# Kernel optimization log

Hardware: AMD Instinct MI355X
Metric: run time of the kernel (lower is better)

Reference implementation:

```python
import jax, jax.numpy as jnp
import numpy as np

DIM = 1024
DEPTH = 8
DIM_HEAD = 64
HEADS = 16
NUM_Q = 16
EMB = 768
OUT = 1024
FF_INNER = 4 * DIM
INNER = DIM_HEAD * HEADS  # 1024
B, N1 = 64, 577
EPS = 1e-5


def _ln(x, g, b):
    mu = jnp.mean(x, axis=-1, keepdims=True)
    var = jnp.mean((x - mu) ** 2, axis=-1, keepdims=True)
    return (x - mu) * jax.lax.rsqrt(var + EPS) * g + b


def setup_inputs() -> dict:
    key = jax.random.key(0)
    ks = jax.random.split(key, 16)
    std = 0.02
    inp = {
        'x': jax.random.normal(ks[0], (B, N1, EMB), jnp.float32),
        'queries': jax.random.normal(ks[1], (1, NUM_Q, DIM), jnp.float32) / DIM ** 0.5,
        'proj_in_w': jax.random.normal(ks[2], (EMB, DIM), jnp.float32) * std,
        'proj_in_b': jnp.zeros((DIM,), jnp.float32),
        'ln1_g': jnp.ones((DEPTH, DIM), jnp.float32),
        'ln1_b': jnp.zeros((DEPTH, DIM), jnp.float32),
        'ln2_g': jnp.ones((DEPTH, DIM), jnp.float32),
        'ln2_b': jnp.zeros((DEPTH, DIM), jnp.float32),
        'wq': jax.random.normal(ks[3], (DEPTH, DIM, INNER), jnp.float32) * std,
        'wkv': jax.random.normal(ks[4], (DEPTH, DIM, 2 * INNER), jnp.float32) * std,
        'wo': jax.random.normal(ks[5], (DEPTH, INNER, DIM), jnp.float32) * std,
        'ffln_g': jnp.ones((DEPTH, DIM), jnp.float32),
        'ffln_b': jnp.zeros((DEPTH, DIM), jnp.float32),
        'w1': jax.random.normal(ks[6], (DEPTH, DIM, FF_INNER), jnp.float32) * std,
        'w2': jax.random.normal(ks[7], (DEPTH, FF_INNER, DIM), jnp.float32) * std,
        'proj_out_w': jax.random.normal(ks[8], (DIM, OUT), jnp.float32) * std,
        'proj_out_b': jnp.zeros((OUT,), jnp.float32),
        'nout_g': jnp.ones((OUT,), jnp.float32),
        'nout_b': jnp.zeros((OUT,), jnp.float32),
    }
    return inp


def reference(x, queries, proj_in_w, proj_in_b, ln1_g, ln1_b, ln2_g, ln2_b,
              wq, wkv, wo, ffln_g, ffln_b, w1, w2,
              proj_out_w, proj_out_b, nout_g, nout_b):
    b = x.shape[0]
    xp = x @ proj_in_w + proj_in_b          # (b, n1, dim)
    latents0 = jnp.broadcast_to(queries, (b, NUM_Q, DIM))
    scale = DIM_HEAD ** -0.25               # applied to both q and k

    def layer(latents, p):
        (g1, b1, g2, b2, Wq, Wkv, Wo, gf, bf, W1, W2) = p
        xn = _ln(xp, g1, b1)                # (b, n1, dim)
        lt = _ln(latents, g2, b2)           # (b, nq, dim)
        q = lt @ Wq                         # (b, nq, inner)
        kv_in = jnp.concatenate([xn, lt], axis=1)   # (b, n1+nq, dim)
        kv = kv_in @ Wkv                    # (b, n1+nq, 2*inner)
        k, v = jnp.split(kv, 2, axis=-1)
        L = kv_in.shape[1]
        qh = q.reshape(b, NUM_Q, HEADS, DIM_HEAD).transpose(0, 2, 1, 3)
        kh = k.reshape(b, L, HEADS, DIM_HEAD).transpose(0, 2, 1, 3)
        vh = v.reshape(b, L, HEADS, DIM_HEAD).transpose(0, 2, 1, 3)
        logits = jnp.einsum('bhqd,bhkd->bhqk', qh * scale, kh * scale)
        w = jax.nn.softmax(logits.astype(jnp.float32), axis=-1).astype(logits.dtype)
        o = jnp.einsum('bhqk,bhkd->bhqd', w, vh)
        o = o.transpose(0, 2, 1, 3).reshape(b, NUM_Q, INNER) @ Wo
        latents = o + latents
        h = _ln(latents, gf, bf) @ W1
        h = jax.nn.gelu(h, approximate=False)
        latents = h @ W2 + latents
        return latents, None

    params = (ln1_g, ln1_b, ln2_g, ln2_b, wq, wkv, wo, ffln_g, ffln_b, w1, w2)
    latents, _ = jax.lax.scan(layer, latents0, params)
    out = latents @ proj_out_w + proj_out_b
    return _ln(out, nout_g, nout_b)
```

## Files before the change

### kernel.cpp

```cpp
#include <hip/hip_runtime.h>
#include <hip/hip_bf16.h>
#include <math.h>

#define DEV __device__ __forceinline__

typedef __bf16 bf16x8 __attribute__((ext_vector_type(8)));
typedef float f32x4 __attribute__((ext_vector_type(4)));
typedef unsigned short u16x8 __attribute__((ext_vector_type(8)));
typedef unsigned short u16x4 __attribute__((ext_vector_type(4)));

DEV float b2f(unsigned short u){ unsigned int i = ((unsigned int)u)<<16; float f; __builtin_memcpy(&f,&i,4); return f; }
DEV unsigned short f2b(float x){ unsigned int i; __builtin_memcpy(&i,&x,4); unsigned int r = i + 0x7FFFu + ((i>>16)&1u); return (unsigned short)(r>>16); }

DEV int swz(int row, int elem){ return row*64 + ((((elem>>3) ^ row) & 7)<<3) + (elem&7); }

enum { EPI_F32=0, EPI_GELU=2, EPI_RESF32=3 };

__global__ __launch_bounds__(512)
void gemm3(const unsigned short* __restrict__ A, const unsigned short* __restrict__ Bt,
           const float* __restrict__ bias, unsigned short* __restrict__ Out,
           int M, int N, int K, int NT)
{
    __shared__ unsigned short As[256*64];
    __shared__ unsigned short Bs[256*64];
    const int tid  = threadIdx.x;
    const int lane = tid & 63;
    const int wave = tid >> 6;
    const int wr = wave >> 2, wc = wave & 3;
    const int nb = blockIdx.x;
    const int nt = nb % NT, mt = nb / NT;

    f32x4 acc[8][4];
    #pragma unroll
    for (int m=0;m<8;m++)
      #pragma unroll
      for (int n=0;n<4;n++) acc[m][n] = f32x4{0.f,0.f,0.f,0.f};

    const unsigned short* pA[4]; const unsigned short* pB[4];
    int dA[4], dB[4];
    #pragma unroll
    for (int i=0;i<4;i++){
      int e = (i*512+tid)*8; int row = e>>6, col = e&63;
      int gr = mt*256 + row; if (gr > M-1) gr = M-1;
      pA[i] = A + (size_t)gr*K + col;
      dA[i] = swz(row,col);
      pB[i] = Bt + (size_t)(nt*256+row)*K + col;
      dB[i] = swz(row,col);
    }

    u16x8 rA[4], rB[4];
    auto issue = [&](int k0){
      #pragma unroll
      for (int i=0;i<4;i++) rA[i] = *reinterpret_cast<const u16x8*>(pA[i]+k0);
      #pragma unroll
      for (int i=0;i<4;i++) rB[i] = *reinterpret_cast<const u16x8*>(pB[i]+k0);
    };
    auto commit = [&](){
      #pragma unroll
      for (int i=0;i<4;i++) *reinterpret_cast<u16x8*>(&As[dA[i]]) = rA[i];
      #pragma unroll
      for (int i=0;i<4;i++) *reinterpret_cast<u16x8*>(&Bs[dB[i]]) = rB[i];
    };

    issue(0);
    const int nk = K / 64;
    #pragma unroll 1
    for (int kt=0; kt<nk; kt++){
      __syncthreads();
      commit();
      __syncthreads();
      if (kt+1 < nk) issue((kt+1)*64);
      #pragma unroll
      for (int kk=0; kk<2; kk++){
        bf16x8 bv[4];
        #pragma unroll
        for (int n=0;n<4;n++){
          int r = wc*64 + n*16 + (lane&15);
          bv[n] = (bf16x8)(*reinterpret_cast<const u16x8*>(&Bs[swz(r, kk*32 + (lane>>4)*8)]));
        }
        #pragma unroll
        for (int m=0;m<8;m++){
          int r = wr*128 + m*16 + (lane&15);
          bf16x8 av = (bf16x8)(*reinterpret_cast<const u16x8*>(&As[swz(r, kk*32 + (lane>>4)*8)]));
          #pragma unroll
          for (int n=0;n<4;n++)
            acc[m][n] = __builtin_amdgcn_mfma_f32_16x16x32_bf16(av, bv[n], acc[m][n], 0, 0, 0);
        }
      }
    }

    #pragma unroll
    for (int m=0;m<8;m++){
      #pragma unroll
      for (int n=0;n<4;n++){
        #pragma unroll
        for (int r=0;r<4;r++){
          int row = mt*256 + wr*128 + m*16 + (lane>>4)*4 + r;
          int col = nt*256 + wc*64 + n*16 + (lane&15);
          if (row < M){
            float v = acc[m][n][r];
            if (bias) v += bias[col];
            Out[(size_t)row*N + col] = f2b(v);
          }
        }
      }
    }
}

template<int EPI>
__global__ __launch_bounds__(256)
void gemm_sp2(const unsigned short* __restrict__ AH, const unsigned short* __restrict__ AL,
              const unsigned short* __restrict__ BH, const unsigned short* __restrict__ BL,
              const float* __restrict__ bias, const float* __restrict__ Res,
              void* __restrict__ Out, unsigned short* __restrict__ OutL,
              int M, int N, int K, int NT)
{
    constexpr int MR=2, NR=2;
    __shared__ unsigned short As[2*64*64];
    __shared__ unsigned short Bs[2*64*64];
    const int tid  = threadIdx.x;
    const int lane = tid & 63;
    const int wave = tid >> 6;
    const int wr = wave >> 1, wc = wave & 1;
    const int chunk = gridDim.x >> 3;
    const int nb = (blockIdx.x & 7)*chunk + (blockIdx.x >> 3);
    const int nt = nb % NT, mt = nb / NT;

    f32x4 acc[MR][NR];
    #pragma unroll
    for (int m=0;m<MR;m++)
      #pragma unroll
      for (int n=0;n<NR;n++) acc[m][n] = f32x4{0.f,0.f,0.f,0.f};

    const unsigned short *pA[2], *pB[2];
    int dst[2];
    #pragma unroll
    for (int i=0;i<2;i++){
      int e = (i*256+tid)*8; int row = e>>6, col = e&63;
      pA[i] = AH + (size_t)(mt*64+row)*K + col;
      pB[i] = BH + (size_t)(nt*64+row)*K + col;
      dst[i] = swz(row,col);
    }
    const size_t dAL = (size_t)(AL - AH);
    const size_t dBL = (size_t)(BL - BH);

    u16x8 rAH0[2], rAL0[2], rBH0[2], rBL0[2];
    u16x8 rAH1[2], rAL1[2], rBH1[2], rBL1[2];
    auto issue0 = [&](int k0){
      #pragma unroll
      for (int i=0;i<2;i++){
        rAH0[i] = *reinterpret_cast<const u16x8*>(pA[i]+k0);
        rAL0[i] = *reinterpret_cast<const u16x8*>(pA[i]+dAL+k0);
        rBH0[i] = *reinterpret_cast<const u16x8*>(pB[i]+k0);
        rBL0[i] = *reinterpret_cast<const u16x8*>(pB[i]+dBL+k0);
      }
    };
    auto issue1 = [&](int k0){
      #pragma unroll
      for (int i=0;i<2;i++){
        rAH1[i] = *reinterpret_cast<const u16x8*>(pA[i]+k0);
        rAL1[i] = *reinterpret_cast<const u16x8*>(pA[i]+dAL+k0);
        rBH1[i] = *reinterpret_cast<const u16x8*>(pB[i]+k0);
        rBL1[i] = *reinterpret_cast<const u16x8*>(pB[i]+dBL+k0);
      }
    };
    auto commit0 = [&](){
      #pragma unroll
      for (int i=0;i<2;i++){
        *reinterpret_cast<u16x8*>(&As[dst[i]])      = rAH0[i];
        *reinterpret_cast<u16x8*>(&As[4096+dst[i]]) = rAL0[i];
        *reinterpret_cast<u16x8*>(&Bs[dst[i]])      = rBH0[i];
        *reinterpret_cast<u16x8*>(&Bs[4096+dst[i]]) = rBL0[i];
      }
    };
    auto commit1 = [&](){
      #pragma unroll
      for (int i=0;i<2;i++){
        *reinterpret_cast<u16x8*>(&As[dst[i]])      = rAH1[i];
        *reinterpret_cast<u16x8*>(&As[4096+dst[i]]) = rAL1[i];
        *reinterpret_cast<u16x8*>(&Bs[dst[i]])      = rBH1[i];
        *reinterpret_cast<u16x8*>(&Bs[4096+dst[i]]) = rBL1[i];
      }
    };
    auto compute = [&](){
      #pragma unroll
      for (int kk=0; kk<2; kk++){
        bf16x8 ah[MR], al[MR], bh[NR], bl[NR];
        #pragma unroll
        for (int m=0;m<MR;m++){
          int a = swz(wr*32 + m*16 + (lane&15), kk*32 + (lane>>4)*8);
          ah[m] = (bf16x8)(*reinterpret_cast<const u16x8*>(&As[a]));
          al[m] = (bf16x8)(*reinterpret_cast<const u16x8*>(&As[4096 + a]));
        }
        #pragma unroll
        for (int n=0;n<NR;n++){
          int a = swz(wc*32 + n*16 + (lane&15), kk*32 + (lane>>4)*8);
          bh[n] = (bf16x8)(*reinterpret_cast<const u16x8*>(&Bs[a]));
          bl[n] = (bf16x8)(*reinterpret_cast<const u16x8*>(&Bs[4096 + a]));
        }
        #pragma unroll
        for (int m=0;m<MR;m++)
          #pragma unroll
          for (int n=0;n<NR;n++){
            acc[m][n] = __builtin_amdgcn_mfma_f32_16x16x32_bf16(ah[m], bh[n], acc[m][n], 0, 0, 0);
            acc[m][n] = __builtin_amdgcn_mfma_f32_16x16x32_bf16(ah[m], bl[n], acc[m][n], 0, 0, 0);
            acc[m][n] = __builtin_amdgcn_mfma_f32_16x16x32_bf16(al[m], bh[n], acc[m][n], 0, 0, 0);
          }
      }
    };

    const int nk = K / 64;
    issue0(0); issue1(64);
    #pragma unroll 1
    for (int kt=0; kt<nk; kt+=2){
      __syncthreads();
      commit0();
      __syncthreads();
      if (kt+2 < nk) issue0((kt+2)*64);
      compute();
      __syncthreads();
      commit1();
      __syncthreads();
      if (kt+3 < nk) issue1((kt+3)*64);
      compute();
    }

    #pragma unroll
    for (int m=0;m<MR;m++){
      #pragma unroll
      for (int n=0;n<NR;n++){
        #pragma unroll
        for (int r=0;r<4;r++){
          int row = mt*64 + wr*32 + m*16 + (lane>>4)*4 + r;
          int col = nt*64 + wc*32 + n*16 + (lane&15);
          float v = acc[m][n][r];
          if (bias) v += bias[col];
          if constexpr (EPI==EPI_GELU){
            v = 0.5f*v*(1.0f + erff(v*0.70710678118654752f));
            unsigned short hi = f2b(v);
            ((unsigned short*)Out)[(size_t)row*N + col] = hi;
            OutL[(size_t)row*N + col] = f2b(v - b2f(hi));
          } else {
            if constexpr (EPI==EPI_RESF32) v += Res[(size_t)row*N + col];
            ((float*)Out)[(size_t)row*N + col] = v;
          }
        }
      }
    }
}

enum { OM_F32=0, OM_BF16=1, OM_SPLIT=2 };
template<bool INF32, int OM, bool HASGB>
__global__ __launch_bounds__(256)
void ln_rows(const void* __restrict__ In, void* __restrict__ Out,
             unsigned short* __restrict__ OutL,
             const float* __restrict__ g, const float* __restrict__ bb)
{
  const int row = blockIdx.x;
  const int tid = threadIdx.x;
  const size_t base = (size_t)row*1024 + tid*4;
  float v[4];
  if constexpr (INF32){
    f32x4 t = *reinterpret_cast<const f32x4*>((const float*)In + base);
    v[0]=t[0]; v[1]=t[1]; v[2]=t[2]; v[3]=t[3];
  } else {
    u16x4 t = *reinterpret_cast<const u16x4*>((const unsigned short*)In + base);
    #pragma unroll
    for (int j=0;j<4;j++) v[j] = b2f(t[j]);
  }
  float s = v[0]+v[1]+v[2]+v[3];
  float q = v[0]*v[0]+v[1]*v[1]+v[2]*v[2]+v[3]*v[3];
  #pragma unroll
  for (int o=32;o>0;o>>=1){ s += __shfl_xor(s,o,64); q += __shfl_xor(q,o,64); }
  __shared__ float sm[8];
  const int wave = tid>>6, lane = tid&63;
  if (lane==0){ sm[wave] = s; sm[4+wave] = q; }
  __syncthreads();
  s = sm[0]+sm[1]+sm[2]+sm[3];
  q = sm[4]+sm[5]+sm[6]+sm[7];
  const float mean = s*(1.f/1024.f);
  const float rstd = rsqrtf(fmaxf(q*(1.f/1024.f) - mean*mean, 0.f) + 1e-5f);
  #pragma unroll
  for (int j=0;j<4;j++){
    float t2 = (v[j]-mean)*rstd;
    if constexpr (HASGB) t2 = t2*g[tid*4+j] + bb[tid*4+j];
    v[j] = t2;
  }
  if constexpr (OM==OM_F32){
    f32x4 t{v[0],v[1],v[2],v[3]};
    *reinterpret_cast<f32x4*>((float*)Out + base) = t;
  } else if constexpr (OM==OM_BF16){
    u16x4 t{f2b(v[0]),f2b(v[1]),f2b(v[2]),f2b(v[3])};
    *reinterpret_cast<u16x4*>((unsigned short*)Out + base) = t;
  } else {
    u16x4 h{f2b(v[0]),f2b(v[1]),f2b(v[2]),f2b(v[3])};
    u16x4 l{f2b(v[0]-b2f(h[0])),f2b(v[1]-b2f(h[1])),f2b(v[2]-b2f(h[2])),f2b(v[3]-b2f(h[3]))};
    *reinterpret_cast<u16x4*>((unsigned short*)Out + base) = h;
    *reinterpret_cast<u16x4*>(OutL + base) = l;
  }
}

template<bool LO>
__global__ __launch_bounds__(256)
void transpose_cvt_b(const float* __restrict__ W, const float* __restrict__ rs,
                     unsigned short* __restrict__ Wt, unsigned short* __restrict__ Wtlo,
                     int K, int N, size_t wLS, size_t tLS, int dstRowOff)
{
  const int l = blockIdx.z;
  const float* Wl = W + (size_t)l*wLS;
  __shared__ float t[32][33];
  const int tx = threadIdx.x & 31, ty = threadIdx.x >> 5;
  const int n0 = blockIdx.x*32, k0 = blockIdx.y*32;
  #pragma unroll
  for (int j=0;j<4;j++){
    int r = ty + j*8;
    float w = Wl[(size_t)(k0+r)*N + n0 + tx];
    if (rs) w *= rs[l*1024 + k0+r];
    t[r][tx] = w;
  }
  __syncthreads();
  #pragma unroll
  for (int j=0;j<4;j++){
    int r = ty + j*8;
    float w = t[tx][r];
    unsigned short hi = f2b(w);
    size_t di = (size_t)l*tLS + (size_t)(dstRowOff + n0 + r)*K + k0 + tx;
    Wt[di] = hi;
    if constexpr (LO) Wtlo[di] = f2b(w - b2f(hi));
  }
}

__global__ __launch_bounds__(256)
void biaskv_kernel(const float* __restrict__ ln1b, const float* __restrict__ wkv,
                   float* __restrict__ out)
{
  const int l = blockIdx.y;
  const int n = blockIdx.x*256 + threadIdx.x;
  const float* b1 = ln1b + l*1024;
  const float* W  = wkv + (size_t)l*1024*2048;
  float s = 0.f;
  for (int k=0;k<1024;k++) s += b1[k]*W[(size_t)k*2048 + n];
  out[l*2048 + n] = s;
}

__global__ __launch_bounds__(256)
void init_latents(const float* __restrict__ Q, float* __restrict__ L)
{
  size_t idx = ((size_t)blockIdx.x*256 + threadIdx.x)*4;
  int row = (int)(idx >> 10);
  int col = (int)(idx & 1023);
  f32x4 t = *reinterpret_cast<const f32x4*>(Q + (size_t)(row & 15)*1024 + col);
  *reinterpret_cast<f32x4*>(L + idx) = t;
}

__global__ __launch_bounds__(256)
void cvt_f32_bf16(const float* __restrict__ In, unsigned short* __restrict__ Out, size_t n4)
{
  size_t i = (size_t)blockIdx.x*256 + threadIdx.x;
  if (i >= n4) return;
  f32x4 t = *reinterpret_cast<const f32x4*>(In + i*4);
  u16x4 u{f2b(t[0]),f2b(t[1]),f2b(t[2]),f2b(t[3])};
  *reinterpret_cast<u16x4*>(Out + i*4) = u;
}

__global__ __launch_bounds__(256)
void cvt_f32b_pair(const float* __restrict__ In, unsigned short* __restrict__ Oh,
                   unsigned short* __restrict__ Ol)
{
  size_t idx = ((size_t)blockIdx.x*256 + threadIdx.x)*4;
  f32x4 t = *reinterpret_cast<const f32x4*>(In + idx);
  u16x4 h{f2b(t[0]),f2b(t[1]),f2b(t[2]),f2b(t[3])};
  u16x4 l{f2b(t[0]-b2f(h[0])),f2b(t[1]-b2f(h[1])),f2b(t[2]-b2f(h[2])),f2b(t[3]-b2f(h[3]))};
  *reinterpret_cast<u16x4*>(Oh + idx) = h;
  *reinterpret_cast<u16x4*>(Ol + idx) = l;
}

__global__ __launch_bounds__(256)
void attn_kernel(const float* __restrict__ QKVf,
                 const unsigned short* __restrict__ KVX,
                 unsigned short* __restrict__ ATTOh,
                 unsigned short* __restrict__ ATTOl)
{
  __shared__ float qs[16][64];
  __shared__ float ws[16][600];
  const int tid = threadIdx.x;
  const int bh = blockIdx.x;
  const int b = bh >> 4, h = bh & 15;

  {
    int idx = tid*4;
    int qi = idx >> 6, d = idx & 63;
    f32x4 t = *reinterpret_cast<const f32x4*>(QKVf + (size_t)(b*16+qi)*3072 + h*64 + d);
    #pragma unroll
    for (int j=0;j<4;j++) qs[qi][d+j] = 0.125f * t[j];
  }
  __syncthreads();

  for (int r = tid; r < 593; r += 256){
    float a[16];
    #pragma unroll
    for (int qi=0;qi<16;qi++) a[qi] = 0.f;
    if (r < 577){
      const unsigned short* krow = KVX + ((size_t)(b*577 + r)*2048 + h*64);
      #pragma unroll 4
      for (int d4=0; d4<16; d4++){
        u16x4 k4 = *reinterpret_cast<const u16x4*>(krow + d4*4);
        float kf0=b2f(k4[0]), kf1=b2f(k4[1]), kf2=b2f(k4[2]), kf3=b2f(k4[3]);
        #pragma unroll
        for (int qi=0;qi<16;qi++){
          f32x4 q4 = *reinterpret_cast<const f32x4*>(&qs[qi][d4*4]);
          a[qi] += q4[0]*kf0 + q4[1]*kf1 + q4[2]*kf2 + q4[3]*kf3;
        }
      }
    } else {
      const float* krow = QKVf + (size_t)(b*16 + (r-577))*3072 + 1024 + h*64;
      #pragma unroll 4
      for (int d4=0; d4<16; d4++){
        f32x4 k4 = *reinterpret_cast<const f32x4*>(krow + d4*4);
        #pragma unroll
        for (int qi=0;qi<16;qi++){
          f32x4 q4 = *reinterpret_cast<const f32x4*>(&qs[qi][d4*4]);
          a[qi] += q4[0]*k4[0] + q4[1]*k4[1] + q4[2]*k4[2] + q4[3]*k4[3];
        }
      }
    }
    #pragma unroll
    for (int qi=0;qi<16;qi++) ws[qi][r] = a[qi];
  }
  __syncthreads();

  const int wave = tid>>6, lane = tid&63;
  for (int qi = wave; qi < 16; qi += 4){
    float m = -1e30f;
    for (int r = lane; r < 593; r += 64) m = fmaxf(m, ws[qi][r]);
    #pragma unroll
    for (int o=32;o>0;o>>=1) m = fmaxf(m, __shfl_xor(m,o,64));
    float s = 0.f;
    for (int r = lane; r < 593; r += 64){ float e = expf(ws[qi][r]-m); ws[qi][r] = e; s += e; }
    #pragma unroll
    for (int o=32;o>0;o>>=1) s += __shfl_xor(s,o,64);
    float inv = 1.f/s;
    for (int r = lane; r < 593; r += 64) ws[qi][r] *= inv;
  }
  __syncthreads();

  const int d = tid & 63, qg = tid >> 6;
  float o0=0.f,o1=0.f,o2=0.f,o3=0.f;
  for (int rr=0; rr<576; rr+=4){
    f32x4 w0 = *reinterpret_cast<const f32x4*>(&ws[qg   ][rr]);
    f32x4 w1 = *reinterpret_cast<const f32x4*>(&ws[qg+4 ][rr]);
    f32x4 w2 = *reinterpret_cast<const f32x4*>(&ws[qg+8 ][rr]);
    f32x4 w3 = *reinterpret_cast<const f32x4*>(&ws[qg+12][rr]);
    #pragma unroll
    for (int j=0;j<4;j++){
      const unsigned short* vrow = KVX + ((size_t)(b*577 + rr + j)*2048 + 1024 + h*64);
      float v = b2f(vrow[d]);
      o0 += w0[j]*v; o1 += w1[j]*v; o2 += w2[j]*v; o3 += w3[j]*v;
    }
  }
  {
    float v = b2f(KVX[(size_t)(b*577 + 576)*2048 + 1024 + h*64 + d]);
    o0 += ws[qg][576]*v; o1 += ws[qg+4][576]*v; o2 += ws[qg+8][576]*v; o3 += ws[qg+12][576]*v;
  }
  for (int r=577; r<593; r++){
    float v = QKVf[(size_t)(b*16 + (r-577))*3072 + 2048 + h*64 + d];
    o0 += ws[qg][r]*v; o1 += ws[qg+4][r]*v; o2 += ws[qg+8][r]*v; o3 += ws[qg+12][r]*v;
  }
  float ov[4] = {o0,o1,o2,o3};
  #pragma unroll
  for (int j=0;j<4;j++){
    size_t idx = (size_t)(b*16+qg+4*j)*1024 + h*64 + d;
    unsigned short hi = f2b(ov[j]);
    ATTOh[idx] = hi;
    ATTOl[idx] = f2b(ov[j] - b2f(hi));
  }
}

extern "C" void kernel_launch(void* const* d_in, const int* in_sizes, int n_in,
                              void* d_out, int out_size, void* d_ws, size_t ws_size,
                              hipStream_t stream)
{
  const float* x    = (const float*)d_in[0];
  const float* qry  = (const float*)d_in[1];
  const float* piw  = (const float*)d_in[2];
  const float* pib  = (const float*)d_in[3];
  const float* ln1g = (const float*)d_in[4];
  const float* ln1b = (const float*)d_in[5];
  const float* ln2g = (const float*)d_in[6];
  const float* ln2b = (const float*)d_in[7];
  const float* wq   = (const float*)d_in[8];
  const float* wkv  = (const float*)d_in[9];
  const float* wo   = (const float*)d_in[10];
  const float* ffg  = (const float*)d_in[11];
  const float* ffb  = (const float*)d_in[12];
  const float* w1   = (const float*)d_in[13];
  const float* w2   = (const float*)d_in[14];
  const float* pow_ = (const float*)d_in[15];
  const float* pob  = (const float*)d_in[16];
  const float* ng   = (const float*)d_in[17];
  const float* nb   = (const float*)d_in[18];

  const int MROWS = 64*577;
  char* wsb = (char*)d_ws;
  size_t off = 0;
  auto alloc = [&](size_t bytes)->char*{
    char* p = wsb + off; off = (off + bytes + 255) & ~(size_t)255; return p;
  };
  unsigned short* XB     = (unsigned short*)alloc((size_t)36992*768*2);
  unsigned short* XP     = (unsigned short*)alloc((size_t)36992*1024*2);
  unsigned short* KVX    = (unsigned short*)alloc((size_t)36992*2048*2);
  unsigned short* WpiT   = (unsigned short*)alloc((size_t)1024*768*2);
  unsigned short* WkvTs  = (unsigned short*)alloc((size_t)8*2048*1024*2);
  unsigned short* WqkvT  = (unsigned short*)alloc((size_t)8*3072*1024*2);
  unsigned short* WqkvTl = (unsigned short*)alloc((size_t)8*3072*1024*2);
  unsigned short* WoT    = (unsigned short*)alloc((size_t)8*1024*1024*2);
  unsigned short* WoTl   = (unsigned short*)alloc((size_t)8*1024*1024*2);
  unsigned short* W1T    = (unsigned short*)alloc((size_t)4096*1024*2);
  unsigned short* W1Tl   = (unsigned short*)alloc((size_t)4096*1024*2);
  unsigned short* W2T    = (unsigned short*)alloc((size_t)1024*4096*2);
  unsigned short* W2Tl   = (unsigned short*)alloc((size_t)1024*4096*2);
  float*          BKV    = (float*)alloc((size_t)8*2048*4);
  unsigned short* LTh    = (unsigned short*)alloc((size_t)1024*1024*2);
  unsigned short* LTl    = (unsigned short*)alloc((size_t)1024*1024*2);
  float*          QKVf   = (float*)alloc((size_t)1024*3072*4);
  unsigned short* ATTOh  = (unsigned short*)alloc((size_t)1024*1024*2);
  unsigned short* ATTOl  = (unsigned short*)alloc((size_t)1024*1024*2);
  unsigned short* FFHh   = (unsigned short*)alloc((size_t)1024*4096*2);
  unsigned short* FFHl   = (unsigned short*)alloc((size_t)1024*4096*2);
  unsigned short* LATBh  = (unsigned short*)alloc((size_t)1024*1024*2);
  unsigned short* LATBl  = (unsigned short*)alloc((size_t)1024*1024*2);
  float*          LATF   = (float*)alloc((size_t)1024*1024*4);
  if (off > ws_size) return;

  dim3 blk(256);
  dim3 blk5(512);

  cvt_f32_bf16<<<dim3((36928*768/4 + 255)/256), blk, 0, stream>>>(x, XB, (size_t)36928*768/4);
  transpose_cvt_b<false><<<dim3(32,24,1), blk, 0, stream>>>(piw, nullptr, WpiT, nullptr, 768, 1024, 0, 0, 0);
  transpose_cvt_b<false><<<dim3(64,32,8), blk, 0, stream>>>(wkv, ln1g, WkvTs, nullptr, 1024, 2048, (size_t)1024*2048, (size_t)2048*1024, 0);
  transpose_cvt_b<true ><<<dim3(32,32,8), blk, 0, stream>>>(wq,  nullptr, WqkvT, WqkvTl, 1024, 1024, (size_t)1024*1024, (size_t)3072*1024, 0);
  transpose_cvt_b<true ><<<dim3(64,32,8), blk, 0, stream>>>(wkv, nullptr, WqkvT, WqkvTl, 1024, 2048, (size_t)1024*2048, (size_t)3072*1024, 1024);
  transpose_cvt_b<true ><<<dim3(32,32,8), blk, 0, stream>>>(wo,  nullptr, WoT, WoTl, 1024, 1024, (size_t)1024*1024, (size_t)1024*1024, 0);
  biaskv_kernel<<<dim3(8,8), blk, 0, stream>>>(ln1b, wkv, BKV);
  init_latents<<<dim3(1024), blk, 0, stream>>>(qry, LATF);

  gemm3<<<dim3(145*4), blk5, 0, stream>>>(XB, WpiT, pib, XP, MROWS, 1024, 768, 4);
  ln_rows<false,OM_BF16,false><<<dim3(MROWS), blk, 0, stream>>>(XP, XP, nullptr, nullptr, nullptr);

  for (int l=0; l<8; l++){
    transpose_cvt_b<true><<<dim3(128,32,1), blk, 0, stream>>>(w1 + (size_t)l*1024*4096, nullptr, W1T, W1Tl, 1024, 4096, 0, 0, 0);
    transpose_cvt_b<true><<<dim3(32,128,1), blk, 0, stream>>>(w2 + (size_t)l*4096*1024, nullptr, W2T, W2Tl, 4096, 1024, 0, 0, 0);

    ln_rows<true,OM_SPLIT,true><<<dim3(1024), blk, 0, stream>>>(LATF, LTh, LTl, ln2g + l*1024, ln2b + l*1024);
    gemm_sp2<EPI_F32><<<dim3(16*48), blk, 0, stream>>>(
        LTh, LTl, WqkvT + (size_t)l*3072*1024, WqkvTl + (size_t)l*3072*1024,
        nullptr, nullptr, QKVf, nullptr, 1024, 3072, 1024, 48);
    gemm3<<<dim3(145*8), blk5, 0, stream>>>(
        XP, WkvTs + (size_t)l*2048*1024, BKV + l*2048, KVX, MROWS, 2048, 1024, 8);
    attn_kernel<<<dim3(1024), blk, 0, stream>>>(QKVf, KVX, ATTOh, ATTOl);
    gemm_sp2<EPI_RESF32><<<dim3(16*16), blk, 0, stream>>>(
        ATTOh, ATTOl, WoT + (size_t)l*1024*1024, WoTl + (size_t)l*1024*1024,
        nullptr, LATF, LATF, nullptr, 1024, 1024, 1024, 16);
    ln_rows<true,OM_SPLIT,true><<<dim3(1024), blk, 0, stream>>>(LATF, LTh, LTl, ffg + l*1024, ffb + l*1024);
    gemm_sp2<EPI_GELU><<<dim3(16*64), blk, 0, stream>>>(
        LTh, LTl, W1T, W1Tl, nullptr, nullptr, FFHh, FFHl, 1024, 4096, 1024, 64);
    gemm_sp2<EPI_RESF32><<<dim3(16*16), blk, 0, stream>>>(
        FFHh, FFHl, W2T, W2Tl, nullptr, LATF, LATF, nullptr, 1024, 1024, 4096, 16);
  }

  transpose_cvt_b<true><<<dim3(32,32,1), blk, 0, stream>>>(pow_, nullptr, W1T, W1Tl, 1024, 1024, 0, 0, 0);
  cvt_f32b_pair<<<dim3(1024), blk, 0, stream>>>(LATF, LATBh, LATBl);
  gemm_sp2<EPI_F32><<<dim3(16*16), blk, 0, stream>>>(
      LATBh, LATBl, W1T, W1Tl, pob, nullptr, QKVf, nullptr, 1024, 1024, 1024, 16);
  ln_rows<true,OM_F32,true><<<dim3(1024), blk, 0, stream>>>(QKVf, d_out, nullptr, ng, nb);
}
```

Baseline: 5.084 ms.

## Double-buffer GEMM LDS with direct global-to-LDS loads and XCD block swizzle

```diff
diff --git a/kernel.cpp b/kernel.cpp
--- a/kernel.cpp
+++ b/kernel.cpp
@@ -14,6 +14,12 @@
 
 DEV int swz(int row, int elem){ return row*64 + ((((elem>>3) ^ row) & 7)<<3) + (elem&7); }
 
+DEV int xcd_swz(int orig, int nwg){
+  int q = nwg >> 3, r = nwg & 7;
+  int x = orig & 7, idx = orig >> 3;
+  return (x < r ? x*(q+1) : r*(q+1) + (x-r)*q) + idx;
+}
+
 enum { EPI_F32=0, EPI_GELU=2, EPI_RESF32=3 };
 
 __global__ __launch_bounds__(512)
@@ -21,14 +27,16 @@
            const float* __restrict__ bias, unsigned short* __restrict__ Out,
            int M, int N, int K, int NT)
 {
-    __shared__ unsigned short As[256*64];
-    __shared__ unsigned short Bs[256*64];
+    __shared__ unsigned short As[2][256*64];
+    __shared__ unsigned short Bs[2][256*64];
     const int tid  = threadIdx.x;
     const int lane = tid & 63;
     const int wave = tid >> 6;
     const int wr = wave >> 2, wc = wave & 3;
-    const int nb = blockIdx.x;
+    const int nb = xcd_swz(blockIdx.x, gridDim.x);
     const int nt = nb % NT, mt = nb / NT;
+    const int lr = lane >> 3;
+    const int lc = lane & 7;
 
     f32x4 acc[8][4];
     #pragma unroll
@@ -37,56 +45,60 @@
       for (int n=0;n<4;n++) acc[m][n] = f32x4{0.f,0.f,0.f,0.f};
 
     const unsigned short* pA[4]; const unsigned short* pB[4];
-    int dA[4], dB[4];
     #pragma unroll
     for (int i=0;i<4;i++){
-      int e = (i*512+tid)*8; int row = e>>6, col = e&63;
+      int s = wave*4 + i;
+      int row = s*8 + lr;
+      int col = ((lc ^ row)&7)<<3;
       int gr = mt*256 + row; if (gr > M-1) gr = M-1;
       pA[i] = A + (size_t)gr*K + col;
-      dA[i] = swz(row,col);
       pB[i] = Bt + (size_t)(nt*256+row)*K + col;
-      dB[i] = swz(row,col);
-    }
-
-    u16x8 rA[4], rB[4];
-    auto issue = [&](int k0){
-      #pragma unroll
-      for (int i=0;i<4;i++) rA[i] = *reinterpret_cast<const u16x8*>(pA[i]+k0);
-      #pragma unroll
-      for (int i=0;i<4;i++) rB[i] = *reinterpret_cast<const u16x8*>(pB[i]+k0);
+    }
+
+    auto stage = [&](int buf, int k0){
+      #pragma unroll
+      for (int i=0;i<4;i++){
+        int s = wave*4 + i;
+        __builtin_amdgcn_global_load_lds((const unsigned int*)(pA[i]+k0), (unsigned int*)&As[buf][s*512], 16, 0, 0);
+      }
+      #pragma unroll
+      for (int i=0;i<4;i++){
+        int s = wave*4 + i;
+        __builtin_amdgcn_global_load_lds((const unsigned int*)(pB[i]+k0), (unsigned int*)&Bs[buf][s*512], 16, 0, 0);
+      }
     };
-    auto commit = [&](){
-      #pragma unroll
-      for (int i=0;i<4;i++) *reinterpret_cast<u16x8*>(&As[dA[i]]) = rA[i];
-      #pragma unroll
-      for (int i=0;i<4;i++) *reinterpret_cast<u16x8*>(&Bs[dB[i]]) = rB[i];
-    };
-
-    issue(0);
+
+    stage(0, 0);
+    asm volatile("s_waitcnt vmcnt(0)" ::: "memory");
+    __builtin_amdgcn_s_barrier();
+
     const int nk = K / 64;
     #pragma unroll 1
     for (int kt=0; kt<nk; kt++){
-      __syncthreads();
-      commit();
-      __syncthreads();
-      if (kt+1 < nk) issue((kt+1)*64);
+      const int cur = kt & 1;
+      if (kt+1 < nk) stage(cur^1, (kt+1)*64);
+      __builtin_amdgcn_sched_barrier(0);
+      __builtin_amdgcn_s_setprio(1);
       #pragma unroll
       for (int kk=0; kk<2; kk++){
         bf16x8 bv[4];
         #pragma unroll
         for (int n=0;n<4;n++){
           int r = wc*64 + n*16 + (lane&15);
-          bv[n] = (bf16x8)(*reinterpret_cast<const u16x8*>(&Bs[swz(r, kk*32 + (lane>>4)*8)]));
+          bv[n] = (bf16x8)(*reinterpret_cast<const u16x8*>(&Bs[cur][swz(r, kk*32 + (lane>>4)*8)]));
         }
         #pragma unroll
         for (int m=0;m<8;m++){
           int r = wr*128 + m*16 + (lane&15);
-          bf16x8 av = (bf16x8)(*reinterpret_cast<const u16x8*>(&As[swz(r, kk*32 + (lane>>4)*8)]));
+          bf16x8 av = (bf16x8)(*reinterpret_cast<const u16x8*>(&As[cur][swz(r, kk*32 + (lane>>4)*8)]));
           #pragma unroll
           for (int n=0;n<4;n++)
             acc[m][n] = __builtin_amdgcn_mfma_f32_16x16x32_bf16(av, bv[n], acc[m][n], 0, 0, 0);
         }
       }
+      __builtin_amdgcn_s_setprio(0);
+      asm volatile("s_waitcnt vmcnt(0)" ::: "memory");
+      __builtin_amdgcn_s_barrier();
     }
 
     #pragma unroll
```

Result: slower. 5.241 ms (+3.1%).
